# Kernel optimization log

Hardware: AMD Instinct MI355X
Metric: run time of the kernel (lower is better)

Reference implementation:

```python
import jax, jax.numpy as jnp
import numpy as np

IN_F = 4096
OUT_F = 8192
BLOCK = 16   # block_dim
KEEP = 8     # keep_k low-frequency modes kept per block
NLEV = 256   # n_levels


def dct_inv_basis(keep_k, n):
    # Orthonormal DCT-II synthesis basis, rows = kept frequencies k, cols = time index t.
    k = jnp.arange(keep_k, dtype=jnp.float32)[:, None]
    t = jnp.arange(n, dtype=jnp.float32)[None, :]
    B = jnp.cos(jnp.pi * (t + 0.5) * k / n) * jnp.sqrt(2.0 / n)
    scale = jnp.where(jnp.arange(keep_k) == 0, 1.0 / jnp.sqrt(2.0), 1.0)
    return B * scale[:, None]  # [keep_k, block_dim]


def setup_inputs() -> dict:
    key = jax.random.key(0)
    k1, k2, k3, k4, k5 = jax.random.split(key, 5)
    n_blocks = OUT_F * IN_F // BLOCK  # 2097152
    x = jax.random.normal(k1, (32, 8, IN_F), jnp.float32)
    idx = jax.random.randint(k2, (n_blocks, KEEP), 0, NLEV, jnp.int32)
    c_min = jax.random.normal(k3, (KEEP,), jnp.float32)
    c_range = jax.random.uniform(k4, (KEEP,), jnp.float32) + 0.1
    bias = jax.random.normal(k5, (OUT_F,), jnp.float32)
    return {"x": x, "idx": idx, "c_min": c_min, "c_range": c_range, "bias": bias}


def reference(x, idx, c_min, c_range, bias):
    # Affine dequant of kept frequency codes: [n_blocks, keep_k]
    coeffs = idx.astype(jnp.float32) / (NLEV - 1) * c_range + c_min
    # Inverse DCT per block (high-frequency modes are implicitly zero)
    B = dct_inv_basis(KEEP, BLOCK)              # [keep_k, block_dim]
    W = (coeffs @ B).reshape(OUT_F, IN_F)       # dense dequantized weight
    return x @ W.T + bias
```

## Files before the change

kernel.cpp:

```cpp
#include <hip/hip_runtime.h>


typedef __attribute__((ext_vector_type(8))) short bf16x8;
typedef __attribute__((ext_vector_type(4))) float f32x4;

#define K_TOT   2048
#define N_TOT   8192
#define NT      32
#define NCHUNK  8
#define SPC     8
#define LDS_CH  16384

__device__ __forceinline__ unsigned short f2bf_rn(float f) {
    unsigned u = __float_as_uint(f);
    u += 0x7FFFu + ((u >> 16) & 1u);
    return (unsigned short)(u >> 16);
}
__device__ __forceinline__ unsigned pack2(int a, int b) {
    unsigned ua = __float_as_uint((float)a);
    unsigned ub = __float_as_uint((float)b);
    return __builtin_amdgcn_perm(ub, ua, 0x07060302u);
}

__device__ __forceinline__ void lds_barrier() {
    asm volatile("" ::: "memory");
    __builtin_amdgcn_s_waitcnt(0xC07F);
    __builtin_amdgcn_s_barrier();
    asm volatile("" ::: "memory");
}

__global__ __launch_bounds__(256) void prep_kernel(
    const float* __restrict__ x, const float* __restrict__ c_min,
    const float* __restrict__ c_range, unsigned short* __restrict__ Y2f,
    float* __restrict__ corr)
{
    __shared__ float Bk[8][16];
    __shared__ float scmin[8];
    __shared__ float ss[8];
    __shared__ float red[4];
    const int tid = threadIdx.x;
    const int m = blockIdx.x;
    if (tid < 128) {
        int k = tid >> 4, t = tid & 15;
        float v = cosf(3.14159265358979f * (t + 0.5f) * (float)k / 16.0f)
                  * 0.353553390593274f;
        if (k == 0) v *= 0.707106781186548f;
        Bk[k][t] = v;
    }
    if (tid < 8) {
        scmin[tid] = c_min[tid];
        ss[tid] = c_range[tid] * (1.0f / 255.0f);
    }
    __syncthreads();

    const float* xp = x + (long)m * 4096 + tid * 16;
    float xs[16];
#pragma unroll
    for (int q = 0; q < 4; ++q) {
        float4 v = *(const float4*)(xp + q * 4);
        xs[q * 4 + 0] = v.x; xs[q * 4 + 1] = v.y;
        xs[q * 4 + 2] = v.z; xs[q * 4 + 3] = v.w;
    }
    float partial = 0.0f;
    unsigned short yo[8];
#pragma unroll
    for (int k = 0; k < 8; ++k) {
        float y = 0.0f;
#pragma unroll
        for (int t = 0; t < 16; ++t) y += xs[t] * Bk[k][t];
        partial += y * scmin[k];
        yo[k] = f2bf_rn(y * ss[k]);
    }
    uint4 pk;
    pk.x = (unsigned)yo[0] | ((unsigned)yo[1] << 16);
    pk.y = (unsigned)yo[2] | ((unsigned)yo[3] << 16);
    pk.z = (unsigned)yo[4] | ((unsigned)yo[5] << 16);
    pk.w = (unsigned)yo[6] | ((unsigned)yo[7] << 16);
    {
        const int mg = m >> 4, fr = m & 15, kc = tid >> 2, fq = tid & 3;
        unsigned short* dst = Y2f + ((long)((mg * 64 + kc) * 64) + fq * 16 + fr) * 8;
        *(uint4*)dst = pk;
    }
#pragma unroll
    for (int off = 32; off > 0; off >>= 1)
        partial += __shfl_down(partial, off, 64);
    if ((tid & 63) == 0) red[tid >> 6] = partial;
    __syncthreads();
    if (tid == 0) corr[m] = red[0] + red[1] + red[2] + red[3];
}

__global__ __launch_bounds__(512, 2) void gemm_kernel(
    const unsigned short* __restrict__ Y2f, const int* __restrict__ idx,
    const float* __restrict__ bias, const float* __restrict__ corr,
    float* __restrict__ out)
{
    __shared__ char lds[NCHUNK * LDS_CH];

    const int tid  = threadIdx.x;
    const int wave = tid >> 6;
    const int lane = tid & 63;
    const int fr   = lane & 15;
    const int fq   = lane >> 4;
    const int o0   = blockIdx.x * NT;

    const int scol = tid >> 4;
    const int skq  = tid & 15;
    const int* sBase = idx + (long)(o0 + scol) * K_TOT + skq * 4;

    const bf16x8* aF[2];
    aF[0] = (const bf16x8*)Y2f + (long)((wave * 2 + 0) * 64) * 64 + lane;
    aF[1] = (const bf16x8*)Y2f + (long)((wave * 2 + 1) * 64) * 64 + lane;

    f32x4 acc[2][2] = {{{0.f,0.f,0.f,0.f},{0.f,0.f,0.f,0.f}},
                       {{0.f,0.f,0.f,0.f},{0.f,0.f,0.f,0.f}}};
    int4 S[2][4];

#define STAGE_LOAD(ch)                                                    \
    {                                                                     \
        _Pragma("unroll")                                                 \
        for (int r = 0; r < 4; ++r)                                       \
            S[(ch) & 1][r] = *(const int4*)(sBase + (ch) * 256 + r * 64); \
    }

#define STAGE_WRITE(ch)                                                   \
    {                                                                     \
        char* buf = lds + (ch) * LDS_CH;                                  \
        _Pragma("unroll")                                                 \
        for (int r = 0; r < 4; ++r) {                                     \
            const int kq = skq + r * 16;                                  \
            uint2 w;                                                      \
            w.x = pack2(S[(ch) & 1][r].x, S[(ch) & 1][r].y);              \
            w.y = pack2(S[(ch) & 1][r].z, S[(ch) & 1][r].w);              \
            *(uint2*)(buf + scol * 512 + (((kq >> 1) ^ scol) * 16)        \
                      + (kq & 1) * 8) = w;                                \
        }                                                                 \
    }

#define BREAD(buf, s, g)                                                  \
    (*(const bf16x8*)((buf) + (g * 16 + fr) * 512 +                       \
                      ((((s) * 4 + fq) ^ (g * 16 + fr)) * 16)))

    STAGE_LOAD(0)
    STAGE_LOAD(1)
    STAGE_WRITE(0)
    lds_barrier();

#pragma unroll
    for (int c = 0; c < NCHUNK; ++c) {
        bf16x8 a[SPC][2];
#pragma unroll
        for (int s = 0; s < SPC; ++s) {
            a[s][0] = aF[0][(c * SPC + s) * 64];
            a[s][1] = aF[1][(c * SPC + s) * 64];
        }
        if (c + 2 < NCHUNK) STAGE_LOAD(c + 2)
        if (c + 1 < NCHUNK) STAGE_WRITE(c + 1)
        lds_barrier();
        {
            const char* buf = lds + c * LDS_CH;
            bf16x8 b[2][2];
            b[0][0] = BREAD(buf, 0, 0);
            b[0][1] = BREAD(buf, 0, 1);
#pragma unroll
            for (int s = 0; s < SPC; ++s) {
                if (s + 1 < SPC) {
                    b[(s + 1) & 1][0] = BREAD(buf, (s + 1), 0);
                    b[(s + 1) & 1][1] = BREAD(buf, (s + 1), 1);
                }
#pragma unroll
                for (int mt = 0; mt < 2; ++mt)
#pragma unroll
                    for (int g = 0; g < 2; ++g)
                        acc[mt][g] = __builtin_amdgcn_mfma_f32_16x16x32_bf16(
                            a[s][mt], b[s & 1][g], acc[mt][g], 0, 0, 0);
            }
        }
    }

#pragma unroll
    for (int mt = 0; mt < 2; ++mt) {
#pragma unroll
        for (int g = 0; g < 2; ++g) {
            const int col = o0 + g * 16 + fr;
            const float bv = bias[col];
            const int row0 = (wave * 2 + mt) * 16 + fq * 4;
#pragma unroll
            for (int r = 0; r < 4; ++r)
                out[(long)(row0 + r) * N_TOT + col] =
                    acc[mt][g][r] + bv + corr[row0 + r];
        }
    }
#undef STAGE_LOAD
#undef STAGE_WRITE
#undef BREAD
}

extern "C" void kernel_launch(void* const* d_in, const int* in_sizes, int n_in,
                              void* d_out, int out_size, void* d_ws, size_t ws_size,
                              hipStream_t stream) {
    const float* x       = (const float*)d_in[0];
    const int*   idx     = (const int*)d_in[1];
    const float* c_min   = (const float*)d_in[2];
    const float* c_range = (const float*)d_in[3];
    const float* bias    = (const float*)d_in[4];
    float* out = (float*)d_out;

    unsigned short* Y2f = (unsigned short*)d_ws;
    float* corr = (float*)((char*)d_ws + (size_t)256 * K_TOT * 2);

    prep_kernel<<<256, 256, 0, stream>>>(x, c_min, c_range, Y2f, corr);
    gemm_kernel<<<256, 512, 0, stream>>>(Y2f, idx, bias, corr, out);
}
```

Baseline: 119.6 us.

## Fuse prep and GEMM into one cooperative kernel with grid sync

Merges the activation DCT-projection prep kernel and the dequant GEMM into a single cooperative kernel. Each block starts its idx prefetch, computes one row of projected activations and its correction term, then waits on a grid-wide sync before running the GEMM. The intent is to remove the second kernel launch and to overlap the first idx loads with the prep work. In exchange it adds the cost of a grid barrier and cooperative-launch overhead, and it depends on all 256 blocks being co-resident.

```diff
diff --git a/kernel.cpp b/kernel.cpp
--- a/kernel.cpp
+++ b/kernel.cpp
@@ -1,4 +1,7 @@
 #include <hip/hip_runtime.h>
+#include <hip/hip_cooperative_groups.h>
+
+namespace cg = cooperative_groups;
 
 
 typedef __attribute__((ext_vector_type(8))) short bf16x8;
@@ -29,90 +32,30 @@
     asm volatile("" ::: "memory");
 }
 
-__global__ __launch_bounds__(256) void prep_kernel(
-    const float* __restrict__ x, const float* __restrict__ c_min,
-    const float* __restrict__ c_range, unsigned short* __restrict__ Y2f,
-    float* __restrict__ corr)
+__global__ __launch_bounds__(512, 2) void fused_kernel(
+    const float* __restrict__ x, const int* __restrict__ idx,
+    const float* __restrict__ c_min, const float* __restrict__ c_range,
+    const float* __restrict__ bias, unsigned short* __restrict__ Y2f,
+    float* __restrict__ corr, float* __restrict__ out)
 {
+    __shared__ char lds[NCHUNK * LDS_CH];
     __shared__ float Bk[8][16];
     __shared__ float scmin[8];
     __shared__ float ss[8];
-    __shared__ float red[4];
-    const int tid = threadIdx.x;
-    const int m = blockIdx.x;
-    if (tid < 128) {
-        int k = tid >> 4, t = tid & 15;
-        float v = cosf(3.14159265358979f * (t + 0.5f) * (float)k / 16.0f)
-                  * 0.353553390593274f;
-        if (k == 0) v *= 0.707106781186548f;
-        Bk[k][t] = v;
-    }
-    if (tid < 8) {
-        scmin[tid] = c_min[tid];
-        ss[tid] = c_range[tid] * (1.0f / 255.0f);
-    }
-    __syncthreads();
-
-    const float* xp = x + (long)m * 4096 + tid * 16;
-    float xs[16];
-#pragma unroll
-    for (int q = 0; q < 4; ++q) {
-        float4 v = *(const float4*)(xp + q * 4);
-        xs[q * 4 + 0] = v.x; xs[q * 4 + 1] = v.y;
-        xs[q * 4 + 2] = v.z; xs[q * 4 + 3] = v.w;
-    }
-    float partial = 0.0f;
-    unsigned short yo[8];
-#pragma unroll
-    for (int k = 0; k < 8; ++k) {
-        float y = 0.0f;
-#pragma unroll
-        for (int t = 0; t < 16; ++t) y += xs[t] * Bk[k][t];
-        partial += y * scmin[k];
-        yo[k] = f2bf_rn(y * ss[k]);
-    }
-    uint4 pk;
-    pk.x = (unsigned)yo[0] | ((unsigned)yo[1] << 16);
-    pk.y = (unsigned)yo[2] | ((unsigned)yo[3] << 16);
-    pk.z = (unsigned)yo[4] | ((unsigned)yo[5] << 16);
-    pk.w = (unsigned)yo[6] | ((unsigned)yo[7] << 16);
-    {
-        const int mg = m >> 4, fr = m & 15, kc = tid >> 2, fq = tid & 3;
-        unsigned short* dst = Y2f + ((long)((mg * 64 + kc) * 64) + fq * 16 + fr) * 8;
-        *(uint4*)dst = pk;
-    }
-#pragma unroll
-    for (int off = 32; off > 0; off >>= 1)
-        partial += __shfl_down(partial, off, 64);
-    if ((tid & 63) == 0) red[tid >> 6] = partial;
-    __syncthreads();
-    if (tid == 0) corr[m] = red[0] + red[1] + red[2] + red[3];
-}
-
-__global__ __launch_bounds__(512, 2) void gemm_kernel(
-    const unsigned short* __restrict__ Y2f, const int* __restrict__ idx,
-    const float* __restrict__ bias, const float* __restrict__ corr,
-    float* __restrict__ out)
-{
-    __shared__ char lds[NCHUNK * LDS_CH];
+    __shared__ float red[8];
 
     const int tid  = threadIdx.x;
     const int wave = tid >> 6;
     const int lane = tid & 63;
     const int fr   = lane & 15;
     const int fq   = lane >> 4;
-    const int o0   = blockIdx.x * NT;
+    const int m    = blockIdx.x;
+    const int o0   = m * NT;
 
     const int scol = tid >> 4;
     const int skq  = tid & 15;
     const int* sBase = idx + (long)(o0 + scol) * K_TOT + skq * 4;
 
-    const bf16x8* aF[2];
-    aF[0] = (const bf16x8*)Y2f + (long)((wave * 2 + 0) * 64) * 64 + lane;
-    aF[1] = (const bf16x8*)Y2f + (long)((wave * 2 + 1) * 64) * 64 + lane;
-
-    f32x4 acc[2][2] = {{{0.f,0.f,0.f,0.f},{0.f,0.f,0.f,0.f}},
-                       {{0.f,0.f,0.f,0.f},{0.f,0.f,0.f,0.f}}};
     int4 S[2][4];
 
 #define STAGE_LOAD(ch)                                                    \
@@ -142,6 +85,72 @@
 
     STAGE_LOAD(0)
     STAGE_LOAD(1)
+
+    if (tid < 128) {
+        int k = tid >> 4, t = tid & 15;
+        float v = cosf(3.14159265358979f * (t + 0.5f) * (float)k / 16.0f)
+                  * 0.353553390593274f;
+        if (k == 0) v *= 0.707106781186548f;
+        Bk[k][t] = v;
+    }
+    if (tid < 8) {
+        scmin[tid] = c_min[tid];
+        ss[tid] = c_range[tid] * (1.0f / 255.0f);
+    }
+    __syncthreads();
+
+    float partial = 0.0f;
+    if (tid < 256) {
+        const float* xp = x + (long)m * 4096 + tid * 16;
+        float xs[16];
+#pragma unroll
+        for (int q = 0; q < 4; ++q) {
+            float4 v = *(const float4*)(xp + q * 4);
+            xs[q * 4 + 0] = v.x; xs[q * 4 + 1] = v.y;
+            xs[q * 4 + 2] = v.z; xs[q * 4 + 3] = v.w;
+        }
+        unsigned short yo[8];
+#pragma unroll
+        for (int k = 0; k < 8; ++k) {
+            float y = 0.0f;
+#pragma unroll
+            for (int t = 0; t < 16; ++t) y += xs[t] * Bk[k][t];
+            partial += y * scmin[k];
+            yo[k] = f2bf_rn(y * ss[k]);
+        }
+        uint4 pk;
+        pk.x = (unsigned)yo[0] | ((unsigned)yo[1] << 16);
+        pk.y = (unsigned)yo[2] | ((unsigned)yo[3] << 16);
+        pk.z = (unsigned)yo[4] | ((unsigned)yo[5] << 16);
+        pk.w = (unsigned)yo[6] | ((unsigned)yo[7] << 16);
+        const int mg = m >> 4, frm = m & 15, kc = tid >> 2, fqp = tid & 3;
+        unsigned short* dst =
+            Y2f + ((long)((mg * 64 + kc) * 64) + fqp * 16 + frm) * 8;
+        *(uint4*)dst = pk;
+    }
+#pragma unroll
+    for (int off = 32; off > 0; off >>= 1)
+        partial += __shfl_down(partial, off, 64);
+    if (lane == 0) red[wave] = partial;
+    __syncthreads();
+    if (tid == 0) {
+        float csum = 0.0f;
+#pragma unroll
+        for (int i = 0; i < 8; ++i) csum += red[i];
+        corr[m] = csum;
+    }
+
+    __threadfence();
+    cg::this_grid().sync();
+    __threadfence();
+
+    const bf16x8* aF[2];
+    aF[0] = (const bf16x8*)Y2f + (long)((wave * 2 + 0) * 64) * 64 + lane;
+    aF[1] = (const bf16x8*)Y2f + (long)((wave * 2 + 1) * 64) * 64 + lane;
+
+    f32x4 acc[2][2] = {{{0.f,0.f,0.f,0.f},{0.f,0.f,0.f,0.f}},
+                       {{0.f,0.f,0.f,0.f},{0.f,0.f,0.f,0.f}}};
+
     STAGE_WRITE(0)
     lds_barrier();
 
@@ -208,6 +217,8 @@
     unsigned short* Y2f = (unsigned short*)d_ws;
     float* corr = (float*)((char*)d_ws + (size_t)256 * K_TOT * 2);
 
-    prep_kernel<<<256, 256, 0, stream>>>(x, c_min, c_range, Y2f, corr);
-    gemm_kernel<<<256, 512, 0, stream>>>(Y2f, idx, bias, corr, out);
-}
+    void* args[] = {(void*)&x, (void*)&idx, (void*)&c_min, (void*)&c_range,
+                    (void*)&bias, (void*)&Y2f, (void*)&corr, (void*)&out};
+    hipLaunchCooperativeKernel((const void*)fused_kernel, dim3(256), dim3(512),
+                               args, 0, stream);
+}
```

Result: slower. 237.8 us (+98.9%).
